# Kernel tuning notes

Hardware: AMD Instinct MI355X
Metric: run time of the kernel (lower is better)

## Reference

```python
import jax, jax.numpy as jnp
from jax import lax
import numpy as np

EPS = 1e-5
NH = 16  # attention heads (c // 16 with c = 256)


def _qconv(x, mod, phase, padding=0, groups=1):
    """Quaternion conv: real weight = modulus * cos(phase), applied per quaternion component.
    x: (B, C, Q, H, W) -> (B, O, Q, H, W)"""
    w = mod * jnp.cos(phase)
    B, C, Qd, H, W = x.shape
    xr = jnp.transpose(x, (0, 2, 1, 3, 4)).reshape(B * Qd, C, H, W)
    y = lax.conv_general_dilated(xr, w, (1, 1), [(padding, padding)] * 2,
                                 dimension_numbers=('NCHW', 'OIHW', 'NCHW'),
                                 feature_group_count=groups)
    O, Ho, Wo = y.shape[1], y.shape[2], y.shape[3]
    return jnp.transpose(y.reshape(B, Qd, O, Ho, Wo), (0, 2, 1, 3, 4))


def _bn(x):
    # IQBN/VQBN: per-channel normalization over (batch, quaternion, spatial), no affine
    m = x.mean(axis=(0, 2, 3, 4), keepdims=True)
    v = x.var(axis=(0, 2, 3, 4), keepdims=True)
    return (x - m) * lax.rsqrt(v + EPS)


def _attn(x, qkv_m, qkv_p, aproj_m, aproj_p, pe_m, pe_p):
    # QAttention: per-component multi-head self-attention over spatial tokens
    B, C, Qd, H, W = x.shape
    kd = C // NH
    qkv = _qconv(x, qkv_m, qkv_p)  # (B, 3C, Q, H, W)
    q, k, v = jnp.split(qkv, 3, axis=1)
    q = q.reshape(B, NH, kd, Qd, H * W)
    k = k.reshape(B, NH, kd, Qd, H * W)
    v = v.reshape(B, NH, kd, Qd, H * W)
    scores = jnp.einsum('bhcqn,bhcqm->bhqnm', q, k) * (kd ** -0.5)
    a = jax.nn.softmax(scores, axis=-1)
    out = jnp.einsum('bhqnm,bhdqm->bhdqn', a, v).reshape(B, C, Qd, H, W)
    # proj + depthwise positional conv on the input
    return _qconv(out, aproj_m, aproj_p) + _qconv(x, pe_m, pe_p, padding=1, groups=C)


def _psa(x, qkv_m, qkv_p, aproj_m, aproj_p, pe_m, pe_p, ffn1_m, ffn1_p, ffn2_m, ffn2_p):
    a = _attn(x, qkv_m, qkv_p, aproj_m, aproj_p, pe_m, pe_p) + x  # attn shortcut
    h = jax.nn.relu(_bn(_qconv(a, ffn1_m, ffn1_p)))
    f = _bn(_qconv(h, ffn2_m, ffn2_p))
    return f + a  # ffn shortcut


def _msab(x, guide, ec_m, ec_p, gl_w, gl_b, mproj_m, mproj_p):
    # MaxSigmoidAttnBlock (nh=1): global sigmoid gate per (batch, quaternion component)
    B, C, Qd, H, W = x.shape
    e = jax.nn.relu(_bn(_qconv(x, ec_m, ec_p)))  # (B, ec, Q, H, W)
    g = guide @ gl_w.T + gl_b                     # (B, ec)
    ec = g.shape[-1]
    a = jnp.einsum('bcqhw,bc->bq', e, g) / jnp.sqrt(jnp.asarray(ec * H * W, jnp.float32))
    a = jax.nn.sigmoid(a)  # scale param = 1.0 (scale=False)
    e = e * a[:, None, :, None, None]
    return jax.nn.relu(_bn(_qconv(e, mproj_m, mproj_p, padding=1)))


def _forward(x, guide, cv1_m, cv1_p, qkv_m, qkv_p, aproj_m, aproj_p, pe_m, pe_p,
             ffn1_m, ffn1_p, ffn2_m, ffn2_p, ec_m, ec_p, gl_w, gl_b,
             mproj_m, mproj_p, cv2_m, cv2_p):
    y = jax.nn.relu(_bn(_qconv(x, cv1_m, cv1_p)))       # (B, 2c, Q, H, W)
    a, b = jnp.split(y, 2, axis=1)                       # each (B, c, Q, H, W)
    p = _psa(b, qkv_m, qkv_p, aproj_m, aproj_p, pe_m, pe_p,
             ffn1_m, ffn1_p, ffn2_m, ffn2_p)
    m = _msab(p, guide, ec_m, ec_p, gl_w, gl_b, mproj_m, mproj_p)
    cat = jnp.concatenate([a, b, p, m], axis=1)          # (B, 4c, Q, H, W)
    return jax.nn.relu(_bn(_qconv(cat, cv2_m, cv2_p)))   # (B, c2, Q, H, W)


def setup_inputs():
    B, C1, Qd, H, W = 2, 512, 4, 24, 24
    c = 256; ecd = 128; gc = 512; C2 = 512
    ks = jax.random.split(jax.random.key(0), 24)
    def rp(k, shape, s=0.02):
        return s * jax.random.normal(k, shape, dtype=jnp.float32)
    return {
        'x': jax.random.normal(ks[0], (B, C1, Qd, H, W), dtype=jnp.float32),
        'guide': jax.random.normal(ks[1], (B, gc), dtype=jnp.float32),
        'cv1_m': rp(ks[2], (2 * c, C1, 1, 1)),
        'cv1_p': rp(ks[3], (2 * c, C1, 1, 1), 0.1),
        'qkv_m': rp(ks[4], (3 * c, c, 1, 1)),
        'qkv_p': rp(ks[5], (3 * c, c, 1, 1), 0.1),
        'aproj_m': rp(ks[6], (c, c, 1, 1)),
        'aproj_p': rp(ks[7], (c, c, 1, 1), 0.1),
        'pe_m': rp(ks[8], (c, 1, 3, 3)),
        'pe_p': rp(ks[9], (c, 1, 3, 3), 0.1),
        'ffn1_m': rp(ks[10], (2 * c, c, 1, 1)),
        'ffn1_p': rp(ks[11], (2 * c, c, 1, 1), 0.1),
        'ffn2_m': rp(ks[12], (c, 2 * c, 1, 1)),
        'ffn2_p': rp(ks[13], (c, 2 * c, 1, 1), 0.1),
        'ec_m': rp(ks[14], (ecd, c, 1, 1)),
        'ec_p': rp(ks[15], (ecd, c, 1, 1), 0.1),
        'gl_w': rp(ks[16], (ecd, gc), 0.05),
        'gl_b': jnp.zeros((ecd,), dtype=jnp.float32),
        'mproj_m': rp(ks[17], (c, ecd, 3, 3)),
        'mproj_p': rp(ks[18], (c, ecd, 3, 3), 0.1),
        'cv2_m': rp(ks[19], (C2, 4 * c, 1, 1)),
        'cv2_p': rp(ks[20], (C2, 4 * c, 1, 1), 0.1),
    }


def reference(x, guide, cv1_m, cv1_p, qkv_m, qkv_p, aproj_m, aproj_p, pe_m, pe_p,
              ffn1_m, ffn1_p, ffn2_m, ffn2_p, ec_m, ec_p, gl_w, gl_b,
              mproj_m, mproj_p, cv2_m, cv2_p):
    return _forward(x, guide, cv1_m, cv1_p, qkv_m, qkv_p, aproj_m, aproj_p, pe_m, pe_p,
                    ffn1_m, ffn1_p, ffn2_m, ffn2_p, ec_m, ec_p, gl_w, gl_b,
                    mproj_m, mproj_p, cv2_m, cv2_p)
```

## Files before the change

kernel.cpp:

```cpp
#include <hip/hip_runtime.h>
#include <math.h>

typedef __bf16 bf16x8 __attribute__((ext_vector_type(8)));
typedef float f32x4 __attribute__((ext_vector_type(4)));
typedef unsigned short u16;
typedef unsigned int u32;

__device__ __forceinline__ u16 f2bf(float f) {
  u32 u = __float_as_uint(f);
  u32 r = u + 0x7FFF + ((u >> 16) & 1);
  return (u16)(r >> 16);
}
__device__ __forceinline__ float bf2f(u16 h) { return __uint_as_float(((u32)h) << 16); }

static constexpr size_t OB_WBF = 0;
static constexpr size_t OB_WPE = 3276800;
static constexpr size_t OB_ST  = 3286016;
static constexpr size_t OB_GV  = 3310592;
static constexpr size_t OB_GACC= 3311616;
static constexpr size_t OB_CAT = 3311872;
static constexpr size_t OB_YA  = OB_CAT + 9437184;
static constexpr size_t OB_U1  = OB_YA + 9437184;
static constexpr size_t OB_U2  = OB_U1 + 4718592;
static constexpr size_t OB_U3  = OB_U2 + 14155776;
static constexpr size_t OB_AOB = OB_U3 + 4718592;
static constexpr size_t OB_A1B = OB_AOB + 2359296;
static constexpr size_t WS_TOTAL = OB_A1B + 2359296;

struct HeadP {
  const float* m[8]; const float* p[8]; u16* wout;
  const float* pem; const float* pep; float* peout;
  const float* x; u16* xb;
  const float* guide; const float* glw; const float* glb; float* gv;
  int cum[9]; int nwp;
};
__global__ __launch_bounds__(256) void k_head(HeadP P) {
  int bid = blockIdx.x;
  if (bid < P.nwp) {
    int i = bid * 256 + threadIdx.x;
    if (i < 2304) {
      int tap = i >> 8, c = i & 255;
      P.peout[i] = P.pem[c * 9 + tap] * cosf(P.pep[c * 9 + tap]);
    }
    if (i >= P.cum[8]) return;
    int s = 0;
    while (s < 7 && i >= P.cum[s + 1]) s++;
    int j = i - P.cum[s];
    int src = j;
    if (s == 6) {
      int o = j / 1152, r = j % 1152, kk = r >> 7, cc = r & 127;
      src = (o * 128 + cc) * 9 + kk;
    }
    P.wout[i] = f2bf(P.m[s][src] * cosf(P.p[s][src]));
    return;
  }
  bid -= P.nwp;
  if (bid < 2304) {
    int mt = bid % 18; bid /= 18;
    int ct = bid % 16; bid /= 16;
    int q = bid & 3, b = bid >> 2;
    __shared__ float tile[32][33];
    int tj = threadIdx.x & 31, ti = threadIdx.x >> 5;
    const float* xp = P.x + (((size_t)(b * 512 + ct * 32) * 4 + q) * 576) + mt * 32;
#pragma unroll
    for (int ii = 0; ii < 4; ii++)
      tile[ti + ii * 8][tj] = xp[(size_t)(ti + ii * 8) * 4 * 576 + tj];
    __syncthreads();
    u16* yp = P.xb + ((size_t)b * 2304 + q * 576 + mt * 32) * 512 + ct * 32;
#pragma unroll
    for (int mm = 0; mm < 4; mm++)
      yp[(size_t)(mm * 8 + ti) * 512 + tj] = f2bf(tile[tj][mm * 8 + ti]);
    return;
  }
  bid -= 2304;
  int wv = threadIdx.x >> 6, lane = threadIdx.x & 63;
  int be = bid * 4 + wv;
  int b = be >> 7, e = be & 127;
  const float* gr = P.guide + b * 512;
  const float* wr = P.glw + e * 512;
  float s = 0.f;
  for (int c = lane; c < 512; c += 64) s = fmaf(gr[c], wr[c], s);
#pragma unroll
  for (int off = 32; off > 0; off >>= 1) s += __shfl_down(s, off, 64);
  if (lane == 0) P.gv[be] = s + P.glb[e];
}

struct GemmP {
  const u16* W; const u16* X; float* Y; u16* Yb; float* St;
  const u16* CAT; const float* W9;
  const float* EF; const float* GA;
  long long xOff[8];
  int lda, O, K, M, G;
};

template <int BM, int NWO, int WO, int WM, int MODE>
__global__ __launch_bounds__(256) void k_gemm(GemmP P) {
  constexpr int FO = WO / 16, FM = WM / 16;
  constexpr int ABYTES = 16384, BBYTES = BM * 128;
  __shared__ __align__(16) char lds[2 * ABYTES + 2 * BBYTES];
  const int mt = P.M / BM;
  const int ot = P.O >> 7;
  int bid = blockIdx.x;
  const int g = bid / (mt * ot);
  const int rr = bid % (mt * ot);
  const int ob = (rr / mt) << 7;
  const int mb = (rr % mt) * BM;
  const int t = threadIdx.x, lane = t & 63, wave = t >> 6;
  const int wo = (wave % NWO) * WO, wm = (wave / NWO) * WM;
  const u16* Wp = P.W + (size_t)ob * P.K;
  const u16* Xp = (MODE == 2) ? nullptr : (P.X + P.xOff[g] + (size_t)mb * P.lda);

  float gt = 0.f;
  int bq2304 = 0;
  if constexpr (MODE == 2) {
    bq2304 = (g >> 2) * 2304 + (g & 3) * 576;
    float a = P.GA[g] / sqrtf(73728.0f);
    gt = 1.f / (1.f + __expf(-a));
  }

  f32x4 acc[FO][FM] = {};
  float vreg[2][8];

  auto stageA = [&](int tb, int k0) {
#pragma unroll
    for (int i = 0; i < 4; i++) {
      int s = (i * 4 + wave) * 64 + lane;
      int row = s >> 3;
      int kg = (s & 7) ^ (row & 7);
      const u16* src = Wp + (size_t)row * P.K + k0 + kg * 8;
      __builtin_amdgcn_global_load_lds(
          (const __attribute__((address_space(1))) u32*)src,
          (__attribute__((address_space(3))) u32*)(lds + tb * ABYTES + (size_t)(i * 4 + wave) * 1024),
          16, 0, 0);
    }
  };
  auto stageB = [&](int tb, int k0) {
#pragma unroll
    for (int i = 0; i < BM * 8 / 256; i++) {
      int s = (i * 4 + wave) * 64 + lane;
      int row = s >> 3;
      int kg = (s & 7) ^ (row & 7);
      const u16* src = Xp + (size_t)row * P.lda + k0 + kg * 8;
      __builtin_amdgcn_global_load_lds(
          (const __attribute__((address_space(1))) u32*)src,
          (__attribute__((address_space(3))) u32*)(lds + 2 * ABYTES + tb * BBYTES +
                                                   (size_t)(i * 4 + wave) * 1024),
          16, 0, 0);
    }
  };
  auto loadEF = [&](int k0) {
#pragma unroll
    for (int i = 0; i < 2; i++) {
      int s = t + i * 256;
      int row = s >> 3, kg = s & 7;
      int k = k0 + kg * 8;
      int kk = k >> 7, cc = k & 127;
      int n = mb + row;
      int h = n / 24 + kk / 3 - 1, w = n % 24 + kk % 3 - 1;
      if (h >= 0 && h < 24 && w >= 0 && w < 24) {
        const float* ep = P.EF + ((size_t)(bq2304 + h * 24 + w)) * 128 + cc;
        f32x4 v0 = *(const f32x4*)ep;
        f32x4 v1 = *(const f32x4*)(ep + 4);
#pragma unroll
        for (int j = 0; j < 4; j++) { vreg[i][j] = v0[j]; vreg[i][4 + j] = v1[j]; }
      } else {
#pragma unroll
        for (int j = 0; j < 8; j++) vreg[i][j] = 0.f;
      }
    }
  };
  auto writeB = [&](int tb) {
#pragma unroll
    for (int i = 0; i < 2; i++) {
      int s = t + i * 256;
      int row = s >> 3, kg = s & 7;
      u16 pk[8];
#pragma unroll
      for (int j = 0; j < 8; j++) pk[j] = f2bf(vreg[i][j] * gt);
      *(uint4*)&lds[2 * ABYTES + tb * BBYTES + (((row << 3) + (kg ^ (row & 7))) << 4)] =
          *(uint4*)pk;
    }
  };

  const int nt = P.K >> 6;
  stageA(0, 0);
  if constexpr (MODE != 2) {
    stageB(0, 0);
  } else {
    loadEF(0);
    writeB(0);
  }
  __syncthreads();

  for (int tt = 0; tt < nt; tt++) {
    const int cur = tt & 1, nxt = cur ^ 1;
    const bool more = (tt + 1) < nt;
    if (more) {
      stageA(nxt, (tt + 1) << 6);
      if constexpr (MODE != 2) stageB(nxt, (tt + 1) << 6);
      else loadEF((tt + 1) << 6);
    }
    const char* bA = lds + cur * ABYTES;
    const char* bB = lds + 2 * ABYTES + cur * BBYTES;
#pragma unroll
    for (int kk = 0; kk < 2; kk++) {
      int kgl = kk * 4 + (lane >> 4);
      bf16x8 af[FO], bfm[FM];
#pragma unroll
      for (int fo = 0; fo < FO; fo++) {
        int row = wo + fo * 16 + (lane & 15);
        af[fo] = *(bf16x8*)&bA[((row << 3) + (kgl ^ (row & 7))) << 4];
      }
#pragma unroll
      for (int fm = 0; fm < FM; fm++) {
        int row = wm + fm * 16 + (lane & 15);
        bfm[fm] = *(bf16x8*)&bB[((row << 3) + (kgl ^ (row & 7))) << 4];
      }
#pragma unroll
      for (int fo = 0; fo < FO; fo++)
#pragma unroll
        for (int fm = 0; fm < FM; fm++)
          acc[fo][fm] = __builtin_amdgcn_mfma_f32_16x16x32_bf16(af[fo], bfm[fm], acc[fo][fm], 0, 0, 0);
    }
    if (more) {
      if constexpr (MODE == 2) writeB(nxt);
      __syncthreads();
    }
  }

  size_t ybase = (size_t)g * P.M * P.O;
#pragma unroll
  for (int fo = 0; fo < FO; fo++) {
    int ow = ob + wo + fo * 16 + ((lane >> 4) << 2);
#pragma unroll
    for (int fm = 0; fm < FM; fm++) {
      int m = mb + wm + fm * 16 + (lane & 15);
      f32x4 v = acc[fo][fm];
      if constexpr (MODE == 1) {
        size_t tokc = ((size_t)g * 2304 + m) * 1024 + 256 + ow;
        ushort4 cv = *(const ushort4*)&P.CAT[tokc];
        v[0] += bf2f(cv.x); v[1] += bf2f(cv.y); v[2] += bf2f(cv.z); v[3] += bf2f(cv.w);
        int q_ = m / 576, hw_ = m % 576, h_ = hw_ / 24, w_ = hw_ % 24;
        size_t rowb = ((size_t)g * 2304 + q_ * 576) * 1024 + 256 + ow;
#pragma unroll
        for (int tp = 0; tp < 9; tp++) {
          int hh = h_ + tp / 3 - 1, ww = w_ + tp % 3 - 1;
          if (hh < 0 || hh > 23 || ww < 0 || ww > 23) continue;
          ushort4 tv = *(const ushort4*)&P.CAT[rowb + (size_t)(hh * 24 + ww) * 1024];
          f32x4 wt = *(const f32x4*)&P.W9[tp * 256 + ow];
          v[0] = fmaf(wt[0], bf2f(tv.x), v[0]);
          v[1] = fmaf(wt[1], bf2f(tv.y), v[1]);
          v[2] = fmaf(wt[2], bf2f(tv.z), v[2]);
          v[3] = fmaf(wt[3], bf2f(tv.w), v[3]);
        }
        acc[fo][fm] = v;
      }
      size_t off = ybase + (size_t)m * P.O + ow;
      if (P.Y) *(f32x4*)&P.Y[off] = v;
      if (P.Yb) {
        ushort4 r;
        r.x = f2bf(v[0]); r.y = f2bf(v[1]); r.z = f2bf(v[2]); r.w = f2bf(v[3]);
        *(ushort4*)&P.Yb[off] = r;
      }
    }
  }

  if (P.St) {
#pragma unroll
    for (int fo = 0; fo < FO; fo++) {
      float sv[4], qv[4];
#pragma unroll
      for (int j = 0; j < 4; j++) { sv[j] = 0.f; qv[j] = 0.f; }
#pragma unroll
      for (int fm = 0; fm < FM; fm++)
#pragma unroll
        for (int j = 0; j < 4; j++) {
          float a = acc[fo][fm][j];
          sv[j] += a;
          qv[j] = fmaf(a, a, qv[j]);
        }
#pragma unroll
      for (int j = 0; j < 4; j++) {
#pragma unroll
        for (int mk = 1; mk < 16; mk <<= 1) {
          sv[j] += __shfl_xor(sv[j], mk, 64);
          qv[j] += __shfl_xor(qv[j], mk, 64);
        }
      }
      if ((lane & 15) == 0) {
        int o = ob + wo + fo * 16 + ((lane >> 4) << 2);
#pragma unroll
        for (int j = 0; j < 4; j++) {
          atomicAdd(&P.St[2 * (o + j)], sv[j]);
          atomicAdd(&P.St[2 * (o + j) + 1], qv[j]);
        }
      }
    }
  }
}

struct NormP {
  const float* X; const float* st; const u16* AddB;
  u16* Yb; float* Yf; const float* gv; float* gacc;
  long long ybOff[8];
  int ldyb, O, G, M, relu;
  float n;
};
__global__ __launch_bounds__(256) void k_norm(NormP P) {
  int O4 = P.O >> 2;
  long long idx = (long long)blockIdx.x * 256 + threadIdx.x;
  if (idx >= (long long)P.G * P.M * O4) return;
  int c4 = (int)(idx % O4);
  long long gm = idx / O4;
  int m = (int)(gm % P.M);
  int g = (int)(gm / P.M);
  size_t off = (size_t)gm * P.O + c4 * 4;
  f32x4 v = *(const f32x4*)&P.X[off];
  float inv_n = 1.0f / P.n;
#pragma unroll
  for (int j = 0; j < 4; j++) {
    int c = c4 * 4 + j;
    float mean = P.st[2 * c] * inv_n;
    float var = P.st[2 * c + 1] * inv_n - mean * mean;
    v[j] = (v[j] - mean) * rsqrtf(var + 1e-5f);
  }
  if (P.AddB) {
    ushort4 av = *(const ushort4*)(P.AddB + off);
    v[0] += bf2f(av.x); v[1] += bf2f(av.y); v[2] += bf2f(av.z); v[3] += bf2f(av.w);
  }
  if (P.relu) {
#pragma unroll
    for (int j = 0; j < 4; j++) v[j] = fmaxf(v[j], 0.f);
  }
  if (P.Yb) {
    ushort4 r;
    r.x = f2bf(v[0]); r.y = f2bf(v[1]); r.z = f2bf(v[2]); r.w = f2bf(v[3]);
    *(ushort4*)(P.Yb + P.ybOff[g] + (size_t)m * P.ldyb + c4 * 4) = r;
  }
  if (P.Yf) *(f32x4*)&P.Yf[off] = v;
  if (P.gacc) {
    float gs = 0.f;
#pragma unroll
    for (int j = 0; j < 4; j++) gs = fmaf(v[j], P.gv[g * 128 + c4 * 4 + j], gs);
#pragma unroll
    for (int mk = 1; mk < 64; mk <<= 1) gs += __shfl_xor(gs, mk, 64);
    __shared__ float t1[4];
    int lane = threadIdx.x & 63, wv = threadIdx.x >> 6;
    if (lane == 0) t1[wv] = gs;
    __syncthreads();
    if (threadIdx.x == 0)
      atomicAdd(&P.gacc[g * 4 + m / 576], t1[0] + t1[1] + t1[2] + t1[3]);
  }
}

__global__ __launch_bounds__(256) void k_normT(const float* X, const float* st, float* out) {
  int bid = blockIdx.x;
  int ot = bid & 15;
  int mt = (bid >> 4) % 72;
  int b = bid / 1152;
  int mb = mt * 32, ob = ot * 32;
  __shared__ float tile[32][33];
  int c = threadIdx.x & 31, r = threadIdx.x >> 5;
#pragma unroll
  for (int i = 0; i < 4; i++) {
    int row = r + i * 8;
    tile[row][c] = X[((size_t)b * 2304 + mb + row) * 512 + ob + c];
  }
  __syncthreads();
  float inv_n = 1.0f / 4608.0f;
#pragma unroll
  for (int i = 0; i < 4; i++) {
    int o = ob + r + i * 8;
    float mean = st[2 * o] * inv_n;
    float var = st[2 * o + 1] * inv_n - mean * mean;
    float rs = rsqrtf(var + 1e-5f);
    float v = fmaxf((tile[c][r + i * 8] - mean) * rs, 0.f);
    out[((size_t)(b * 512 + o)) * 2304 + mb + c] = v;
  }
}

__global__ __launch_bounds__(256) void k_attn(const u16* qkv, u16* ao) {
  int bid = blockIdx.x;
  int tq = bid % 3; int u = bid / 3;
  int qd = u & 3; u >>= 2;
  int head = u & 15, b = u >> 4;
  int t = threadIdx.x, lane = t & 63, wv = t >> 6;
  int g = lane >> 4, q = lane & 15;
  size_t tok0 = (size_t)b * 2304 + qd * 576;
  const u16* QKV = qkv + tok0 * 768;

  __shared__ __align__(16) char shm[50176];
  u16* Kl = (u16*)(shm);
  u16* VT = (u16*)(shm + 27648);
  u16* Pl = (u16*)(shm + 46080 + wv * 1024);

  for (int i = t; i < 1152; i += 256) {
    int m = i >> 1, half = i & 1;
    const u16* src = QKV + (size_t)m * 768 + 256 + head * 16 + half * 8;
    u16 tmp[8];
    *(uint4*)tmp = *(const uint4*)src;
    ushort4 lo, hi;
    lo.x = f2bf(bf2f(tmp[0]) * 0.25f); lo.y = f2bf(bf2f(tmp[1]) * 0.25f);
    lo.z = f2bf(bf2f(tmp[2]) * 0.25f); lo.w = f2bf(bf2f(tmp[3]) * 0.25f);
    hi.x = f2bf(bf2f(tmp[4]) * 0.25f); hi.y = f2bf(bf2f(tmp[5]) * 0.25f);
    hi.z = f2bf(bf2f(tmp[6]) * 0.25f); hi.w = f2bf(bf2f(tmp[7]) * 0.25f);
    u16* dst = Kl + m * 24 + half * 8;
    *(ushort4*)dst = lo;
    *(ushort4*)(dst + 4) = hi;
  }
  for (int mm = t; mm < 576; mm += 256) {
    const u16* src = QKV + (size_t)mm * 768 + 512 + head * 16;
    u16 tmp[16];
    *(uint4*)tmp = *(const uint4*)src;
    *(uint4*)(tmp + 8) = *(const uint4*)(src + 8);
    u16* dst = VT + (mm >> 3) * 128 + (mm & 7);
#pragma unroll
    for (int d = 0; d < 16; d++) dst[d * 8] = tmp[d];
  }
  __syncthreads();

#pragma unroll 1
  for (int i = 0; i < 3; i++) {
    int tl = wv * 3 + i;
    int qbase = tq * 192 + tl * 16;
    bf16x8 qf = {};
    if (g < 2)
      qf = *(const bf16x8*)(QKV + (size_t)(qbase + q) * 768 + head * 16 + g * 8);

    f32x4 acc_o = {};
    float ssum = 0.f;

    for (int ch = 0; ch < 18; ch++) {
      int m0 = ch * 32;
      f32x4 s[2];
#pragma unroll
      for (int h = 0; h < 2; h++) {
        bf16x8 kf = {};
        if (g < 2)
          kf = *(const bf16x8*)(Kl + (size_t)(m0 + h * 16 + q) * 24 + g * 8);
        f32x4 z = {};
        s[h] = __builtin_amdgcn_mfma_f32_16x16x32_bf16(kf, qf, z, 0, 0, 0);
      }
#pragma unroll
      for (int h = 0; h < 2; h++) {
        float p0 = __expf(s[h][0]);
        float p1 = __expf(s[h][1]);
        float p2 = __expf(s[h][2]);
        float p3 = __expf(s[h][3]);
        ssum += (p0 + p1) + (p2 + p3);
        ushort4 w;
        w.x = f2bf(p0); w.y = f2bf(p1); w.z = f2bf(p2); w.w = f2bf(p3);
        *(ushort4*)(Pl + ((h * 2 + (g >> 1)) * 16 + q) * 8 + (g & 1) * 4) = w;
      }
      bf16x8 va = *(const bf16x8*)(VT + ((m0 >> 3) + g) * 128 + q * 8);
      bf16x8 pa = *(const bf16x8*)(Pl + (g * 16 + q) * 8);
      acc_o = __builtin_amdgcn_mfma_f32_16x16x32_bf16(va, pa, acc_o, 0, 0, 0);
    }

    ssum += __shfl_xor(ssum, 16, 64);
    ssum += __shfl_xor(ssum, 32, 64);
    float inv = 1.f / ssum;
    u16* op = ao + (tok0 + qbase + q) * 256 + head * 16 + g * 4;
    ushort4 r;
    r.x = f2bf(acc_o[0] * inv);
    r.y = f2bf(acc_o[1] * inv);
    r.z = f2bf(acc_o[2] * inv);
    r.w = f2bf(acc_o[3] * inv);
    *(ushort4*)op = r;
  }
}

extern "C" void kernel_launch(void* const* d_in, const int* in_sizes, int n_in,
                              void* d_out, int out_size, void* d_ws, size_t ws_size,
                              hipStream_t stream) {
  if (ws_size < WS_TOTAL) return;
  char* ws = (char*)d_ws;
  u16* WB = (u16*)(ws + OB_WBF);
  float* WPE = (float*)(ws + OB_WPE);
  float* STB = (float*)(ws + OB_ST);
  float* GV = (float*)(ws + OB_GV);
  float* GACC = (float*)(ws + OB_GACC);
  u16* CATB = (u16*)(ws + OB_CAT);
  float* YA = (float*)(ws + OB_YA);
  u16* XBF = (u16*)(ws + OB_U1);
  u16* QKVB = (u16*)(ws + OB_U2);
  float* EF = (float*)(ws + OB_U2 + 10616832);
  u16* HB = (u16*)(ws + OB_U3);
  u16* AOB = (u16*)(ws + OB_AOB);
  u16* A1B = (u16*)(ws + OB_A1B);
  float* out = (float*)d_out;

  hipMemsetAsync(ws + OB_ST, 0, OB_CAT - OB_ST, stream);

  {
    HeadP p;
    const int mi[8] = {2, 4, 6, 10, 12, 14, 18, 20};
    const int sz[8] = {262144, 196608, 65536, 131072, 131072, 32768, 294912, 524288};
    int c = 0;
    for (int i = 0; i < 8; i++) {
      p.m[i] = (const float*)d_in[mi[i]];
      p.p[i] = (const float*)d_in[mi[i] + 1];
      p.cum[i] = c;
      c += sz[i];
    }
    p.cum[8] = c;
    p.wout = WB;
    p.pem = (const float*)d_in[8];
    p.pep = (const float*)d_in[9];
    p.peout = WPE;
    p.x = (const float*)d_in[0];
    p.xb = XBF;
    p.guide = (const float*)d_in[1];
    p.glw = (const float*)d_in[16];
    p.glb = (const float*)d_in[17];
    p.gv = GV;
    p.nwp = (c + 255) / 256;
    int grid = p.nwp + 2304 + 64;
    k_head<<<grid, 256, 0, stream>>>(p);
  }

  auto gemm = [&](int mode, size_t wOff, int O, int K, int M, int G,
                  const u16* X, long long xs, long long xadd, int lda,
                  float* Y, u16* Yb, int si) {
    GemmP p;
    p.W = WB + wOff; p.X = X; p.Y = Y; p.Yb = Yb;
    p.St = (si >= 0) ? (STB + si * 1024) : nullptr;
    p.CAT = CATB; p.W9 = WPE; p.EF = EF; p.GA = GACC;
    p.lda = lda; p.O = O; p.K = K; p.M = M; p.G = G;
    for (int g = 0; g < 8; g++) p.xOff[g] = (long long)(g < G ? g : 0) * xs + xadd;
    int grid = G * (O / 128) * (M / 64);
    if (mode == 0)
      k_gemm<64, 4, 32, 64, 0><<<grid, 256, 0, stream>>>(p);
    else if (mode == 1)
      k_gemm<64, 4, 32, 64, 1><<<grid, 256, 0, stream>>>(p);
    else
      k_gemm<64, 4, 32, 64, 2><<<grid, 256, 0, stream>>>(p);
  };
  auto norm = [&](const float* X, int si, int O, int G, int M, const u16* AddB,
                  u16* Yb, int ldyb, const long long* ybOff, float* Yf, int relu,
                  const float* gv, float* gacc) {
    NormP p;
    p.X = X; p.st = STB + si * 1024; p.AddB = AddB; p.Yb = Yb; p.Yf = Yf;
    p.gv = gv; p.gacc = gacc;
    p.ldyb = ldyb; p.O = O; p.G = G; p.M = M; p.relu = relu;
    p.n = (float)(G * M);
    for (int g = 0; g < 8; g++) p.ybOff[g] = ybOff ? ybOff[(g < G) ? g : 0] : 0;
    long long total = (long long)G * M * (O / 4);
    k_norm<<<(int)((total + 255) / 256), 256, 0, stream>>>(p);
  };

  gemm(0, 0, 512, 512, 2304, 2, XBF, 2304LL * 512, 0, 512, YA, nullptr, 0);
  { long long yo[2] = {0, 2304LL * 1024};
    norm(YA, 0, 512, 2, 2304, nullptr, CATB, 1024, yo, nullptr, 1, nullptr, nullptr); }

  gemm(0, 262144, 768, 256, 2304, 2, CATB, 2304LL * 1024, 256, 1024, nullptr, QKVB, -1);
  k_attn<<<384, 256, 0, stream>>>(QKVB, AOB);
  gemm(1, 458752, 256, 256, 2304, 2, AOB, 2304LL * 256, 0, 256, nullptr, A1B, -1);

  gemm(0, 524288, 512, 256, 2304, 2, A1B, 2304LL * 256, 0, 256, YA, nullptr, 1);
  { long long yo[2] = {0, 2304LL * 512};
    norm(YA, 1, 512, 2, 2304, nullptr, HB, 512, yo, nullptr, 1, nullptr, nullptr); }

  gemm(0, 655360, 256, 512, 2304, 2, HB, 2304LL * 512, 0, 512, YA, nullptr, 2);
  { long long yo[2] = {512, 2304LL * 1024 + 512};
    norm(YA, 2, 256, 2, 2304, A1B, CATB, 1024, yo, nullptr, 0, nullptr, nullptr); }

  gemm(0, 786432, 128, 256, 2304, 2, CATB, 2304LL * 1024, 512, 1024, YA, nullptr, 3);
  norm(YA, 3, 128, 2, 2304, nullptr, nullptr, 0, nullptr, EF, 1, GV, GACC);

  gemm(2, 819200, 256, 1152, 576, 8, nullptr, 0, 0, 0, YA, nullptr, 4);
  { long long yo[8];
    for (int g = 0; g < 8; g++)
      yo[g] = (long long)(g >> 2) * 2304 * 1024 + (long long)(g & 3) * 576 * 1024 + 768;
    norm(YA, 4, 256, 8, 576, nullptr, CATB, 1024, yo, nullptr, 1, nullptr, nullptr); }

  gemm(0, 1114112, 512, 1024, 2304, 2, CATB, 2304LL * 1024, 0, 1024, YA, nullptr, 5);
  k_normT<<<2304, 256, 0, stream>>>(YA, STB + 5 * 1024, out);
}
```

Baseline: 256.4 us.

## Store GEMM pre-norm outputs in bf16 and shrink GEMM output tile to 64

Pre-normalization GEMM outputs and the gate feature buffer are now stored and read as bf16 instead of fp32. This halves the intermediate traffic between the GEMMs and the norm kernels. Separately, the GEMM block tile drops from 128 to 64 output channels (2x2 waves, each 32x32), which doubles the grid for better CU occupancy. Batch-norm statistics are still accumulated in fp32 from the accumulators, but normalizing the bf16-rounded values adds some precision loss.

After: 340.4 us. 32.8% more time.

```diff
diff --git a/kernel.cpp b/kernel.cpp
--- a/kernel.cpp
+++ b/kernel.cpp
@@ -86,9 +86,9 @@
 }
 
 struct GemmP {
-  const u16* W; const u16* X; float* Y; u16* Yb; float* St;
+  const u16* W; const u16* X; u16* Yb; float* St;
   const u16* CAT; const float* W9;
-  const float* EF; const float* GA;
+  const u16* EF; const float* GA;
   long long xOff[8];
   int lda, O, K, M, G;
 };
@@ -96,14 +96,16 @@
 template <int BM, int NWO, int WO, int WM, int MODE>
 __global__ __launch_bounds__(256) void k_gemm(GemmP P) {
   constexpr int FO = WO / 16, FM = WM / 16;
-  constexpr int ABYTES = 16384, BBYTES = BM * 128;
+  constexpr int BO = NWO * WO * ((4 / NWO) > 0 ? 1 : 1) * 1;
+  constexpr int OBLK = NWO * WO;
+  constexpr int ABYTES = OBLK * 128, BBYTES = BM * 128;
   __shared__ __align__(16) char lds[2 * ABYTES + 2 * BBYTES];
   const int mt = P.M / BM;
-  const int ot = P.O >> 7;
+  const int ot = P.O / OBLK;
   int bid = blockIdx.x;
   const int g = bid / (mt * ot);
   const int rr = bid % (mt * ot);
-  const int ob = (rr / mt) << 7;
+  const int ob = (rr / mt) * OBLK;
   const int mb = (rr % mt) * BM;
   const int t = threadIdx.x, lane = t & 63, wave = t >> 6;
   const int wo = (wave % NWO) * WO, wm = (wave / NWO) * WM;
@@ -123,7 +125,7 @@
 
   auto stageA = [&](int tb, int k0) {
 #pragma unroll
-    for (int i = 0; i < 4; i++) {
+    for (int i = 0; i < OBLK * 8 / 256; i++) {
       int s = (i * 4 + wave) * 64 + lane;
       int row = s >> 3;
       int kg = (s & 7) ^ (row & 7);
@@ -158,11 +160,13 @@
       int n = mb + row;
       int h = n / 24 + kk / 3 - 1, w = n % 24 + kk % 3 - 1;
       if (h >= 0 && h < 24 && w >= 0 && w < 24) {
-        const float* ep = P.EF + ((size_t)(bq2304 + h * 24 + w)) * 128 + cc;
-        f32x4 v0 = *(const f32x4*)ep;
-        f32x4 v1 = *(const f32x4*)(ep + 4);
-#pragma unroll
-        for (int j = 0; j < 4; j++) { vreg[i][j] = v0[j]; vreg[i][4 + j] = v1[j]; }
+        const u16* ep = P.EF + ((size_t)(bq2304 + h * 24 + w)) * 128 + cc;
+        ushort4 v0 = *(const ushort4*)ep;
+        ushort4 v1 = *(const ushort4*)(ep + 4);
+        vreg[i][0] = bf2f(v0.x); vreg[i][1] = bf2f(v0.y);
+        vreg[i][2] = bf2f(v0.z); vreg[i][3] = bf2f(v0.w);
+        vreg[i][4] = bf2f(v1.x); vreg[i][5] = bf2f(v1.y);
+        vreg[i][6] = bf2f(v1.z); vreg[i][7] = bf2f(v1.w);
       } else {
 #pragma unroll
         for (int j = 0; j < 8; j++) vreg[i][j] = 0.f;
@@ -256,12 +260,9 @@
         acc[fo][fm] = v;
       }
       size_t off = ybase + (size_t)m * P.O + ow;
-      if (P.Y) *(f32x4*)&P.Y[off] = v;
-      if (P.Yb) {
-        ushort4 r;
-        r.x = f2bf(v[0]); r.y = f2bf(v[1]); r.z = f2bf(v[2]); r.w = f2bf(v[3]);
-        *(ushort4*)&P.Yb[off] = r;
-      }
+      ushort4 r;
+      r.x = f2bf(v[0]); r.y = f2bf(v[1]); r.z = f2bf(v[2]); r.w = f2bf(v[3]);
+      *(ushort4*)&P.Yb[off] = r;
     }
   }
 
@@ -300,8 +301,8 @@
 }
 
 struct NormP {
-  const float* X; const float* st; const u16* AddB;
-  u16* Yb; float* Yf; const float* gv; float* gacc;
+  const u16* X; const float* st; const u16* AddB;
+  u16* Yb; u16* Yfb; const float* gv; float* gacc;
   long long ybOff[8];
   int ldyb, O, G, M, relu;
   float n;
@@ -315,7 +316,8 @@
   int m = (int)(gm % P.M);
   int g = (int)(gm / P.M);
   size_t off = (size_t)gm * P.O + c4 * 4;
-  f32x4 v = *(const f32x4*)&P.X[off];
+  ushort4 xv = *(const ushort4*)&P.X[off];
+  f32x4 v = {bf2f(xv.x), bf2f(xv.y), bf2f(xv.z), bf2f(xv.w)};
   float inv_n = 1.0f / P.n;
 #pragma unroll
   for (int j = 0; j < 4; j++) {
@@ -332,12 +334,10 @@
 #pragma unroll
     for (int j = 0; j < 4; j++) v[j] = fmaxf(v[j], 0.f);
   }
-  if (P.Yb) {
-    ushort4 r;
-    r.x = f2bf(v[0]); r.y = f2bf(v[1]); r.z = f2bf(v[2]); r.w = f2bf(v[3]);
-    *(ushort4*)(P.Yb + P.ybOff[g] + (size_t)m * P.ldyb + c4 * 4) = r;
-  }
-  if (P.Yf) *(f32x4*)&P.Yf[off] = v;
+  ushort4 r;
+  r.x = f2bf(v[0]); r.y = f2bf(v[1]); r.z = f2bf(v[2]); r.w = f2bf(v[3]);
+  if (P.Yb) *(ushort4*)(P.Yb + P.ybOff[g] + (size_t)m * P.ldyb + c4 * 4) = r;
+  if (P.Yfb) *(ushort4*)(P.Yfb + off) = r;
   if (P.gacc) {
     float gs = 0.f;
 #pragma unroll
@@ -353,7 +353,7 @@
   }
 }
 
-__global__ __launch_bounds__(256) void k_normT(const float* X, const float* st, float* out) {
+__global__ __launch_bounds__(256) void k_normT(const u16* X, const float* st, float* out) {
   int bid = blockIdx.x;
   int ot = bid & 15;
   int mt = (bid >> 4) % 72;
@@ -364,7 +364,7 @@
 #pragma unroll
   for (int i = 0; i < 4; i++) {
     int row = r + i * 8;
-    tile[row][c] = X[((size_t)b * 2304 + mb + row) * 512 + ob + c];
+    tile[row][c] = bf2f(X[((size_t)b * 2304 + mb + row) * 512 + ob + c]);
   }
   __syncthreads();
   float inv_n = 1.0f / 4608.0f;
@@ -481,10 +481,10 @@
   float* GV = (float*)(ws + OB_GV);
   float* GACC = (float*)(ws + OB_GACC);
   u16* CATB = (u16*)(ws + OB_CAT);
-  float* YA = (float*)(ws + OB_YA);
+  u16* YAB = (u16*)(ws + OB_YA);
   u16* XBF = (u16*)(ws + OB_U1);
   u16* QKVB = (u16*)(ws + OB_U2);
-  float* EF = (float*)(ws + OB_U2 + 10616832);
+  u16* EFB = (u16*)(ws + OB_U2 + 10616832);
   u16* HB = (u16*)(ws + OB_U3);
   u16* AOB = (u16*)(ws + OB_AOB);
   u16* A1B = (u16*)(ws + OB_A1B);
@@ -521,26 +521,26 @@
 
   auto gemm = [&](int mode, size_t wOff, int O, int K, int M, int G,
                   const u16* X, long long xs, long long xadd, int lda,
-                  float* Y, u16* Yb, int si) {
+                  u16* Yb, int si) {
     GemmP p;
-    p.W = WB + wOff; p.X = X; p.Y = Y; p.Yb = Yb;
+    p.W = WB + wOff; p.X = X; p.Yb = Yb;
     p.St = (si >= 0) ? (STB + si * 1024) : nullptr;
-    p.CAT = CATB; p.W9 = WPE; p.EF = EF; p.GA = GACC;
+    p.CAT = CATB; p.W9 = WPE; p.EF = EFB; p.GA = GACC;
     p.lda = lda; p.O = O; p.K = K; p.M = M; p.G = G;
     for (int g = 0; g < 8; g++) p.xOff[g] = (long long)(g < G ? g : 0) * xs + xadd;
-    int grid = G * (O / 128) * (M / 64);
+    int grid = G * (O / 64) * (M / 64);
     if (mode == 0)
-      k_gemm<64, 4, 32, 64, 0><<<grid, 256, 0, stream>>>(p);
+      k_gemm<64, 2, 32, 32, 0><<<grid, 256, 0, stream>>>(p);
     else if (mode == 1)
-      k_gemm<64, 4, 32, 64, 1><<<grid, 256, 0, stream>>>(p);
+      k_gemm<64, 2, 32, 32, 1><<<grid, 256, 0, stream>>>(p);
     else
-      k_gemm<64, 4, 32, 64, 2><<<grid, 256, 0, stream>>>(p);
+      k_gemm<64, 2, 32, 32, 2><<<grid, 256, 0, stream>>>(p);
   };
-  auto norm = [&](const float* X, int si, int O, int G, int M, const u16* AddB,
-                  u16* Yb, int ldyb, const long long* ybOff, float* Yf, int relu,
+  auto norm = [&](const u16* X, int si, int O, int G, int M, const u16* AddB,
+                  u16* Yb, int ldyb, const long long* ybOff, u16* Yfb, int relu,
                   const float* gv, float* gacc) {
     NormP p;
-    p.X = X; p.st = STB + si * 1024; p.AddB = AddB; p.Yb = Yb; p.Yf = Yf;
+    p.X = X; p.st = STB + si * 1024; p.AddB = AddB; p.Yb = Yb; p.Yfb = Yfb;
     p.gv = gv; p.gacc = gacc;
     p.ldyb = ldyb; p.O = O; p.G = G; p.M = M; p.relu = relu;
     p.n = (float)(G * M);
@@ -549,31 +549,31 @@
     k_norm<<<(int)((total + 255) / 256), 256, 0, stream>>>(p);
   };
 
-  gemm(0, 0, 512, 512, 2304, 2, XBF, 2304LL * 512, 0, 512, YA, nullptr, 0);
+  gemm(0, 0, 512, 512, 2304, 2, XBF, 2304LL * 512, 0, 512, YAB, 0);
   { long long yo[2] = {0, 2304LL * 1024};
-    norm(YA, 0, 512, 2, 2304, nullptr, CATB, 1024, yo, nullptr, 1, nullptr, nullptr); }
-
-  gemm(0, 262144, 768, 256, 2304, 2, CATB, 2304LL * 1024, 256, 1024, nullptr, QKVB, -1);
+    norm(YAB, 0, 512, 2, 2304, nullptr, CATB, 1024, yo, nullptr, 1, nullptr, nullptr); }
+
+  gemm(0, 262144, 768, 256, 2304, 2, CATB, 2304LL * 1024, 256, 1024, QKVB, -1);
   k_attn<<<384, 256, 0, stream>>>(QKVB, AOB);
-  gemm(1, 458752, 256, 256, 2304, 2, AOB, 2304LL * 256, 0, 256, nullptr, A1B, -1);
-
-  gemm(0, 524288, 512, 256, 2304, 2, A1B, 2304LL * 256, 0, 256, YA, nullptr, 1);
+  gemm(1, 458752, 256, 256, 2304, 2, AOB, 2304LL * 256, 0, 256, A1B, -1);
+
+  gemm(0, 524288, 512, 256, 2304, 2, A1B, 2304LL * 256, 0, 256, YAB, 1);
   { long long yo[2] = {0, 2304LL * 512};
-    norm(YA, 1, 512, 2, 2304, nullptr, HB, 512, yo, nullptr, 1, nullptr, nullptr); }
-
-  gemm(0, 655360, 256, 512, 2304, 2, HB, 2304LL * 512, 0, 512, YA, nullptr, 2);
+    norm(YAB, 1, 512, 2, 2304, nullptr, HB, 512, yo, nullptr, 1, nullptr, nullptr); }
+
+  gemm(0, 655360, 256, 512, 2304, 2, HB, 2304LL * 512, 0, 512, YAB, 2);
   { long long yo[2] = {512, 2304LL * 1024 + 512};
-    norm(YA, 2, 256, 2, 2304, A1B, CATB, 1024, yo, nullptr, 0, nullptr, nullptr); }
-
-  gemm(0, 786432, 128, 256, 2304, 2, CATB, 2304LL * 1024, 512, 1024, YA, nullptr, 3);
-  norm(YA, 3, 128, 2, 2304, nullptr, nullptr, 0, nullptr, EF, 1, GV, GACC);
-
-  gemm(2, 819200, 256, 1152, 576, 8, nullptr, 0, 0, 0, YA, nullptr, 4);
+    norm(YAB, 2, 256, 2, 2304, A1B, CATB, 1024, yo, nullptr, 0, nullptr, nullptr); }
+
+  gemm(0, 786432, 128, 256, 2304, 2, CATB, 2304LL * 1024, 512, 1024, YAB, 3);
+  norm(YAB, 3, 128, 2, 2304, nullptr, nullptr, 0, nullptr, EFB, 1, GV, GACC);
+
+  gemm(2, 819200, 256, 1152, 576, 8, nullptr, 0, 0, 0, YAB, 4);
   { long long yo[8];
     for (int g = 0; g < 8; g++)
       yo[g] = (long long)(g >> 2) * 2304 * 1024 + (long long)(g & 3) * 576 * 1024 + 768;
-    norm(YA, 4, 256, 8, 576, nullptr, CATB, 1024, yo, nullptr, 1, nullptr, nullptr); }
-
-  gemm(0, 1114112, 512, 1024, 2304, 2, CATB, 2304LL * 1024, 0, 1024, YA, nullptr, 5);
-  k_normT<<<2304, 256, 0, stream>>>(YA, STB + 5 * 1024, out);
-}
+    norm(YAB, 4, 256, 8, 576, nullptr, CATB, 1024, yo, nullptr, 1, nullptr, nullptr); }
+
+  gemm(0, 1114112, 512, 1024, 2304, 2, CATB, 2304LL * 1024, 0, 1024, YAB, 5);
+  k_normT<<<2304, 256, 0, stream>>>(YAB, STB + 5 * 1024, out);
+}
```
